# Performance work log

Hardware: AMD Instinct MI355X
Metric: run time of the kernel (lower is better)

## Reference

```python
import jax, jax.numpy as jnp
import numpy as np

NUM_GROUPS = 64  # matches fill_max of ids; all groups present w.h.p. so unique-inverse == ids


def setup_inputs() -> dict:
    key = jax.random.key(0)
    ks = jax.random.split(key, 8)
    B, N, D = 8, 8192, 512
    s = 1.0 / np.sqrt(D)
    return {
        "x": jax.random.normal(ks[0], (B, N, D), dtype=jnp.float32),
        "ids": jax.random.randint(ks[1], (N,), 0, NUM_GROUPS),
        "w1": jax.random.normal(ks[2], (D, D), dtype=jnp.float32) * s,
        "b1": jax.random.normal(ks[3], (D,), dtype=jnp.float32) * s,
        "w2": jax.random.normal(ks[4], (D, D), dtype=jnp.float32) * s,
        "b2": jax.random.normal(ks[5], (D,), dtype=jnp.float32) * s,
        "w3": jax.random.normal(ks[6], (D, D), dtype=jnp.float32) * s,
        "b3": jax.random.normal(ks[7], (D,), dtype=jnp.float32) * s,
    }


def reference(x, ids, w1, b1, w2, b2, w3, b3):
    # x: [B, N, D]; ids: [N] group labels in [0, NUM_GROUPS)
    G = NUM_GROUPS
    a = jnp.einsum('bnd,ed->bne', x, w1) + b1          # linear1 logits
    v = jnp.einsum('bnd,ed->bne', x, w2) + b2          # linear2 values
    # move segment axis to front: [N, B, D]
    aT = jnp.transpose(a, (1, 0, 2))
    vT = jnp.transpose(v, (1, 0, 2))
    # per-group stable softmax along the segment axis
    mx = jax.lax.stop_gradient(jax.ops.segment_max(aT, ids, num_segments=G))  # [G,B,D]
    ex = jnp.exp(aT - mx[ids])
    denom = jax.ops.segment_sum(ex, ids, num_segments=G)                      # [G,B,D]
    wts = ex / denom[ids]                                                     # [N,B,D]
    # weighted scatter-sum of values -> [G, B, D] -> [B, G, D]
    y = jnp.transpose(jax.ops.segment_sum(vT * wts, ids, num_segments=G), (1, 0, 2))
    out = jnp.einsum('bgd,ed->bge', y, w3) + b3        # linear3
    # expand: gather group outputs back to per-element rows -> [B, N, D]
    return out[:, ids]
```

## Files before the change

kernel.cpp:

```cpp
#include <hip/hip_runtime.h>
#include <hip/hip_bf16.h>
#include <math.h>

#define B_ 8
#define N_ 8192
#define D_ 512
#define G_ 64
#define M_ (B_ * N_)

typedef short bf16x8 __attribute__((ext_vector_type(8)));
typedef float f32x4 __attribute__((ext_vector_type(4)));

__device__ __forceinline__ unsigned short f2bf(float f) {
    __hip_bfloat16 h = __float2bfloat16(f);
    return *reinterpret_cast<unsigned short*>(&h);
}
__device__ __forceinline__ void gload_lds16(const void* g, void* l) {
    __builtin_amdgcn_global_load_lds((const __attribute__((address_space(1))) void*)g,
                                     (__attribute__((address_space(3))) void*)l,
                                     16, 0, 0);
}

__global__ __launch_bounds__(256) void cast_xp(const float* __restrict__ x,
                                               const int* __restrict__ perm,
                                               unsigned short* __restrict__ xb) {
    const int total = M_ * 128;
    for (int idx = blockIdx.x * 256 + threadIdx.x; idx < total;
         idx += gridDim.x * 256) {
        const int row = idx >> 7;
        const int q = (idx & 127) * 4;
        const int b = row >> 13;
        const int i = row & 8191;
        const float* src = x + (((size_t)(b << 13) + perm[i]) << 9) + q;
        float4 f = *(const float4*)src;
        ushort4 u;
        u.x = f2bf(f.x); u.y = f2bf(f.y); u.z = f2bf(f.z); u.w = f2bf(f.w);
        *(ushort4*)(xb + ((size_t)row << 9) + q) = u;
    }
}

__global__ __launch_bounds__(256) void cast_w(const float* __restrict__ w1,
                                              const float* __restrict__ b1,
                                              const float* __restrict__ w2,
                                              const float* __restrict__ b2,
                                              unsigned short* __restrict__ wB,
                                              float* __restrict__ biasB) {
    int t = blockIdx.x * 256 + threadIdx.x;
    int idx = t * 4;
    int row = idx >> 9;
    int col = idx & 511;
    const float* src = (row < 512) ? (w1 + (size_t)row * 512 + col)
                                   : (w2 + (size_t)(row - 512) * 512 + col);
    float4 f = *(const float4*)src;
    ushort4 u;
    u.x = f2bf(f.x); u.y = f2bf(f.y); u.z = f2bf(f.z); u.w = f2bf(f.w);
    *(ushort4*)(wB + idx) = u;
    if (t < 1024) biasB[t] = (t < 512) ? b1[t] : b2[t - 512];
}

__global__ __launch_bounds__(256) void bl_hist(const int* __restrict__ ids,
                                               int* __restrict__ counts,
                                               int* __restrict__ stripbase) {
    __shared__ int sid[N_];
    __shared__ int sc[256];
    const int g = blockIdx.x;
    const int t = threadIdx.x;
    for (int i = t; i < N_; i += 256) sid[i] = ids[i];
    __syncthreads();
    int c = 0;
    const int nb = t * 32;
#pragma unroll 8
    for (int k = 0; k < 32; ++k) c += (sid[nb + k] == g) ? 1 : 0;
    sc[t] = c;
    __syncthreads();
    if (t == 0) {
        int run = 0;
        for (int i = 0; i < 256; ++i) { int v = sc[i]; sc[i] = run; run += v; }
        counts[g] = run;
    }
    __syncthreads();
    stripbase[g * 256 + t] = sc[t];
}

__global__ __launch_bounds__(256) void bl_emit(const int* __restrict__ ids,
                                               const int* __restrict__ counts,
                                               const int* __restrict__ stripbase,
                                               int* __restrict__ baseO,
                                               int* __restrict__ fgO,
                                               int* __restrict__ perm) {
    __shared__ int sid[N_];
    __shared__ int sb[G_ + 1];
    __shared__ int sbs;
    const int g = blockIdx.x;
    const int t = threadIdx.x;
    for (int i = t; i < N_; i += 256) sid[i] = ids[i];
    if (t == 0) {
        int a = 0;
        for (int gg = 0; gg < G_; ++gg) { sb[gg] = a; a += counts[gg]; }
        sb[G_] = a;
        sbs = sb[g];
    }
    __syncthreads();
    if (g == 0 && t < G_) {
        baseO[t] = sb[t];
        const int row = t * 128;
        int gg = 0;
        while (gg + 1 < G_ && sb[gg + 1] <= row) ++gg;
        fgO[t] = gg;
    }
    int pos = sbs + stripbase[g * 256 + t];
    const int nb = t * 32;
    for (int k = 0; k < 32; ++k)
        if (sid[nb + k] == g) perm[pos++] = nb + k;
}

__global__ __launch_bounds__(512, 2) void gemm_fused(const unsigned short* __restrict__ xb,
                                                     const unsigned short* __restrict__ wB,
                                                     const float* __restrict__ biasB,
                                                     const int* __restrict__ base,
                                                     const int* __restrict__ fg,
                                                     float* __restrict__ pt) {
    extern __shared__ unsigned short smem[];
    unsigned short* lsA = smem;
    unsigned short* lsB = smem + 32768;

    const int o  = blockIdx.x;
    const int mt = (o & 7) + ((o >> 5) << 3);
    const int nt = (o >> 3) & 3;
    const int b  = mt >> 5;
    const int tlb = (mt & 31) * 2;
    const int c0 = nt * 128;

    const int tid = threadIdx.x;
    const int l = tid & 63;
    const int w = tid >> 6;
    const int wm = w >> 2;
    const int wn = w & 3;
    const int lr = l >> 3;
    const int lslot = l & 7;
    const int fr = l & 15;
    const int kq = l >> 4;
    const int scol = 8 * (lslot ^ lr);

    f32x4 acc[8][4];
#pragma unroll
    for (int i = 0; i < 8; ++i)
#pragma unroll
        for (int j = 0; j < 4; ++j) acc[i][j] = (f32x4){0.f, 0.f, 0.f, 0.f};

    const size_t abase = (((size_t)b << 13) + (size_t)(mt & 31) * 256) << 9;

    auto stageT = [&](int buf, int kt) {
#pragma unroll
        for (int q = 0; q < 4; ++q) {
            const int c = w * 4 + q;
            const int row = c * 8 + lr;
            gload_lds16(xb + abase + ((size_t)row << 9) + kt + scol,
                        lsA + buf * 16384 + c * 512);
        }
#pragma unroll
        for (int q = 0; q < 4; ++q) {
            const int c = w * 4 + q;
            const int srcrow = ((c >> 2) & 1) * 512 + c0 + (c >> 3) * 32
                             + (c & 3) * 8 + lr;
            gload_lds16(wB + ((size_t)srcrow << 9) + kt + scol,
                        lsB + buf * 16384 + c * 512);
        }
    };

    stageT(0, 0);
    __syncthreads();
    int cur = 0;
    for (int t8 = 0; t8 < 8; ++t8) {
        if (t8 < 7) stageT(cur ^ 1, (t8 + 1) * 64);
        const unsigned short* pA = lsA + cur * 16384;
        const unsigned short* pB = lsB + cur * 16384;
        const int ib0 = 8 * (kq ^ (fr & 7));
        const int ib1 = 8 * ((4 + kq) ^ (fr & 7));
        bf16x8 bq0[4], bq1[4];
#pragma unroll
        for (int j = 0; j < 4; ++j) {
            const int brow = (wn * 64 + j * 16 + fr) * 64;
            bq0[j] = *(const bf16x8*)&pB[brow + ib0];
            bq1[j] = *(const bf16x8*)&pB[brow + ib1];
        }
#pragma unroll
        for (int i = 0; i < 8; ++i) {
            const int arow = (wm * 128 + i * 16 + fr) * 64;
            bf16x8 a0 = *(const bf16x8*)&pA[arow + ib0];
            bf16x8 a1 = *(const bf16x8*)&pA[arow + ib1];
#pragma unroll
            for (int j = 0; j < 4; ++j)
                acc[i][j] = __builtin_amdgcn_mfma_f32_16x16x32_bf16(a0, bq0[j], acc[i][j], 0, 0, 0);
#pragma unroll
            for (int j = 0; j < 4; ++j)
                acc[i][j] = __builtin_amdgcn_mfma_f32_16x16x32_bf16(a1, bq1[j], acc[i][j], 0, 0, 0);
        }
        __syncthreads();
        cur ^= 1;
    }

    const int tl = tlb + wm;
    const int fg0 = fg[tl];
    const int bnd0 = (fg0 + 1 < G_) ? base[fg0 + 1] : (1 << 30);
    const int bnd1 = (fg0 + 2 < G_) ? base[fg0 + 2] : (1 << 30);
    const int bnd2 = (fg0 + 3 < G_) ? base[fg0 + 3] : (1 << 30);
    float b1c[2], b2c[2];
#pragma unroll
    for (int j = 0; j < 2; ++j) {
        const int col = c0 + wn * 32 + j * 16 + fr;
        b1c[j] = biasB[col];
        b2c[j] = biasB[512 + col];
    }
    float dp[4][2] = {}, yp[4][2] = {};
    const int rbase = tl * 128 + kq * 4;
#pragma unroll
    for (int i = 0; i < 8; ++i)
#pragma unroll
        for (int rr = 0; rr < 4; ++rr) {
            const int row = rbase + i * 16 + rr;
            const int s = (row >= bnd0) + (row >= bnd1) + (row >= bnd2);
#pragma unroll
            for (int j = 0; j < 2; ++j) {
                const float e = __expf(acc[i][j][rr] + b1c[j]);
                const float ey = e * (acc[i][j + 2][rr] + b2c[j]);
#pragma unroll
                for (int s2 = 0; s2 < 4; ++s2) {
                    dp[s2][j] += (s == s2) ? e : 0.f;
                    yp[s2][j] += (s == s2) ? ey : 0.f;
                }
            }
        }
#pragma unroll
    for (int s2 = 0; s2 < 4; ++s2)
#pragma unroll
        for (int j = 0; j < 2; ++j) {
            dp[s2][j] += __shfl_xor(dp[s2][j], 16);
            dp[s2][j] += __shfl_xor(dp[s2][j], 32);
            yp[s2][j] += __shfl_xor(yp[s2][j], 16);
            yp[s2][j] += __shfl_xor(yp[s2][j], 32);
        }
    if (kq == 0) {
#pragma unroll
        for (int s2 = 0; s2 < 4; ++s2)
#pragma unroll
            for (int j = 0; j < 2; ++j) {
                const int colp = c0 + wn * 32 + j * 16 + fr;
                float2 v = make_float2(dp[s2][j], yp[s2][j]);
                *(float2*)&pt[(((size_t)(b * 64 + tl) * 4 + s2) * 512 + colp) * 2] = v;
            }
    }
}

__global__ __launch_bounds__(256) void combineC(const float* __restrict__ pt,
                                                const int* __restrict__ base,
                                                const int* __restrict__ counts,
                                                const int* __restrict__ fg,
                                                float* __restrict__ y) {
    const int g = blockIdx.x, b = blockIdx.y;
    const int bs = base[g];
    int cnt = counts[g];
    if (cnt == 0) cnt = 1;
    const int t0 = bs >> 7, t1 = (bs + cnt - 1) >> 7;
    for (int c = threadIdx.x; c < 512; c += 256) {
        float d = 0.f, yy = 0.f;
        for (int t = t0; t <= t1; ++t) {
            const int s = g - fg[t];
            if (s >= 0 && s < 4) {
                const float* p = &pt[((((size_t)(b * 64 + t)) * 4 + s) * 512 + c) * 2];
                d += p[0];
                yy += p[1];
            }
        }
        y[((size_t)(b * G_ + g)) * 512 + c] = yy / d;
    }
}

__global__ __launch_bounds__(256) void gemm3(const float* __restrict__ y,
                                             const float* __restrict__ w3,
                                             const float* __restrict__ b3,
                                             float* __restrict__ out_small) {
    __shared__ float ys[16][68];
    __shared__ float wss[16][68];
    const int m0 = blockIdx.x * 64;
    const int n0 = blockIdx.y * 64;
    const int tid = threadIdx.x;
    const int tr = tid >> 4;
    const int tc = tid & 15;
    const int lrow = tid >> 2;
    const int lk4 = (tid & 3) * 4;

    float acc[4][4] = {};

    for (int k0 = 0; k0 < D_; k0 += 16) {
        float4 yv = *(const float4*)(y + (size_t)(m0 + lrow) * D_ + k0 + lk4);
        float4 wv = *(const float4*)(w3 + (size_t)(n0 + lrow) * D_ + k0 + lk4);
        __syncthreads();
        ys[lk4 + 0][lrow] = yv.x;  ys[lk4 + 1][lrow] = yv.y;
        ys[lk4 + 2][lrow] = yv.z;  ys[lk4 + 3][lrow] = yv.w;
        wss[lk4 + 0][lrow] = wv.x; wss[lk4 + 1][lrow] = wv.y;
        wss[lk4 + 2][lrow] = wv.z; wss[lk4 + 3][lrow] = wv.w;
        __syncthreads();
#pragma unroll
        for (int kk = 0; kk < 16; ++kk) {
            float4 y4 = *(const float4*)&ys[kk][tr * 4];
            float4 w4 = *(const float4*)&wss[kk][tc * 4];
            float ya[4] = {y4.x, y4.y, y4.z, y4.w};
            float wa[4] = {w4.x, w4.y, w4.z, w4.w};
#pragma unroll
            for (int i = 0; i < 4; ++i)
#pragma unroll
                for (int j = 0; j < 4; ++j)
                    acc[i][j] = fmaf(ya[i], wa[j], acc[i][j]);
        }
    }

    float bb[4];
#pragma unroll
    for (int j = 0; j < 4; ++j) bb[j] = b3[n0 + tc * 4 + j];
#pragma unroll
    for (int i = 0; i < 4; ++i) {
        size_t o = (size_t)(m0 + tr * 4 + i) * D_ + n0 + tc * 4;
        float4 r;
        r.x = acc[i][0] + bb[0]; r.y = acc[i][1] + bb[1];
        r.z = acc[i][2] + bb[2]; r.w = acc[i][3] + bb[3];
        *(float4*)(out_small + o) = r;
    }
}

__global__ __launch_bounds__(256) void gather_out(const int* __restrict__ ids,
                                                  const float* __restrict__ out_small,
                                                  float* __restrict__ out) {
    const int c = blockIdx.x * 256 + threadIdx.x;
    const int per_row = D_ / 4;
    const int b = c / (N_ * per_row);
    const int rem = c % (N_ * per_row);
    const int n = rem / per_row;
    const int q = rem % per_row;
    const int g = ids[n];
    float4 val = *(const float4*)(out_small + ((size_t)b * G_ + g) * D_ + q * 4);
    *(float4*)(out + (size_t)c * 4) = val;
}

extern "C" void kernel_launch(void* const* d_in, const int* in_sizes, int n_in,
                              void* d_out, int out_size, void* d_ws, size_t ws_size,
                              hipStream_t stream) {
    (void)in_sizes; (void)n_in; (void)out_size; (void)ws_size;
    const float* x   = (const float*)d_in[0];
    const int*   ids = (const int*)d_in[1];
    const float* w1  = (const float*)d_in[2];
    const float* b1  = (const float*)d_in[3];
    const float* w2  = (const float*)d_in[4];
    const float* b2  = (const float*)d_in[5];
    const float* w3  = (const float*)d_in[6];
    const float* b3  = (const float*)d_in[7];
    float* out = (float*)d_out;

    float* ws_f = (float*)d_ws;
    unsigned short* xb = (unsigned short*)ws_f;
    float* after_xb  = ws_f + 16777216;
    unsigned short* wB = (unsigned short*)after_xb;
    float* biasB     = after_xb + 262144;
    float* pt        = biasB + 1024;
    float* y         = pt + 2097152;
    float* out_small = y + 262144;
    int*   perm      = (int*)(out_small + 262144);
    int*   base      = perm + N_;
    int*   counts    = base + G_;
    int*   fg        = counts + G_;
    int*   stripbase = fg + G_;

    hipFuncSetAttribute((const void*)gemm_fused,
                        hipFuncAttributeMaxDynamicSharedMemorySize, 131072);

    hipLaunchKernelGGL(bl_hist, dim3(G_), dim3(256), 0, stream, ids, counts, stripbase);
    hipLaunchKernelGGL(bl_emit, dim3(G_), dim3(256), 0, stream,
                       ids, counts, stripbase, base, fg, perm);
    hipLaunchKernelGGL(cast_w, dim3(512), dim3(256), 0, stream, w1, b1, w2, b2, wB, biasB);
    hipLaunchKernelGGL(cast_xp, dim3(2048), dim3(256), 0, stream, x, perm, xb);
    hipLaunchKernelGGL(gemm_fused, dim3(1024), dim3(512), 131072, stream,
                       xb, wB, biasB, base, fg, pt);
    hipLaunchKernelGGL(combineC, dim3(G_, B_), dim3(256), 0, stream, pt, base, counts, fg, y);
    hipLaunchKernelGGL(gemm3, dim3(8, 8), dim3(256), 0, stream, y, w3, b3, out_small);
    hipLaunchKernelGGL(gather_out, dim3(32768), dim3(256), 0, stream, ids, out_small, out);
}
```

Baseline: 194.9 us.

## Restructure GEMM main loop into ping-pong schedule with explicit vmcnt waits

```diff
diff --git a/kernel.cpp b/kernel.cpp
--- a/kernel.cpp
+++ b/kernel.cpp
@@ -150,13 +150,13 @@
 
     const size_t abase = (((size_t)b << 13) + (size_t)(mt & 31) * 256) << 9;
 
-    auto stageT = [&](int buf, int kt) {
+    auto stage8 = [&](int slot, int kt) {
 #pragma unroll
         for (int q = 0; q < 4; ++q) {
             const int c = w * 4 + q;
             const int row = c * 8 + lr;
             gload_lds16(xb + abase + ((size_t)row << 9) + kt + scol,
-                        lsA + buf * 16384 + c * 512);
+                        lsA + slot * 16384 + c * 512);
         }
 #pragma unroll
         for (int q = 0; q < 4; ++q) {
@@ -164,40 +164,56 @@
             const int srcrow = ((c >> 2) & 1) * 512 + c0 + (c >> 3) * 32
                              + (c & 3) * 8 + lr;
             gload_lds16(wB + ((size_t)srcrow << 9) + kt + scol,
-                        lsB + buf * 16384 + c * 512);
+                        lsB + slot * 16384 + c * 512);
         }
     };
 
-    stageT(0, 0);
-    __syncthreads();
-    int cur = 0;
-    for (int t8 = 0; t8 < 8; ++t8) {
-        if (t8 < 7) stageT(cur ^ 1, (t8 + 1) * 64);
-        const unsigned short* pA = lsA + cur * 16384;
-        const unsigned short* pB = lsB + cur * 16384;
-        const int ib0 = 8 * (kq ^ (fr & 7));
-        const int ib1 = 8 * ((4 + kq) ^ (fr & 7));
-        bf16x8 bq0[4], bq1[4];
-#pragma unroll
-        for (int j = 0; j < 4; ++j) {
-            const int brow = (wn * 64 + j * 16 + fr) * 64;
-            bq0[j] = *(const bf16x8*)&pB[brow + ib0];
-            bq1[j] = *(const bf16x8*)&pB[brow + ib1];
-        }
-#pragma unroll
-        for (int i = 0; i < 8; ++i) {
-            const int arow = (wm * 128 + i * 16 + fr) * 64;
-            bf16x8 a0 = *(const bf16x8*)&pA[arow + ib0];
-            bf16x8 a1 = *(const bf16x8*)&pA[arow + ib1];
-#pragma unroll
-            for (int j = 0; j < 4; ++j)
-                acc[i][j] = __builtin_amdgcn_mfma_f32_16x16x32_bf16(a0, bq0[j], acc[i][j], 0, 0, 0);
-#pragma unroll
-            for (int j = 0; j < 4; ++j)
-                acc[i][j] = __builtin_amdgcn_mfma_f32_16x16x32_bf16(a1, bq1[j], acc[i][j], 0, 0, 0);
-        }
-        __syncthreads();
-        cur ^= 1;
+    stage8(0, 0);
+    stage8(1, 64);
+
+    for (int i4 = 0; i4 < 4; ++i4) {
+#pragma unroll
+        for (int half = 0; half < 2; ++half) {
+            const int slot = half;
+            const bool doStage = (half == 0) ? (i4 > 0) : (i4 < 3);
+            if (doStage) stage8(1 - half, (2 * i4 + 1 + half) * 64);
+            if (doStage || (half == 0)) {
+                asm volatile("s_waitcnt vmcnt(8)" ::: "memory");
+            } else {
+                asm volatile("s_waitcnt vmcnt(0)" ::: "memory");
+            }
+            __builtin_amdgcn_s_barrier();
+
+            const unsigned short* pA = lsA + slot * 16384;
+            const unsigned short* pB = lsB + slot * 16384;
+            bf16x8 bq[4];
+#pragma unroll
+            for (int ks = 0; ks < 2; ++ks) {
+                const int ib = 8 * ((ks * 4 + kq) ^ (fr & 7));
+#pragma unroll
+                for (int ih = 0; ih < 2; ++ih) {
+                    bf16x8 a[4];
+#pragma unroll
+                    for (int i = 0; i < 4; ++i)
+                        a[i] = *(const bf16x8*)&pA[(wm * 128 + (ih * 4 + i) * 16 + fr) * 64 + ib];
+                    if (ih == 0) {
+#pragma unroll
+                        for (int j = 0; j < 4; ++j)
+                            bq[j] = *(const bf16x8*)&pB[(wn * 64 + j * 16 + fr) * 64 + ib];
+                    }
+                    __builtin_amdgcn_s_barrier();
+                    __builtin_amdgcn_s_setprio(1);
+#pragma unroll
+                    for (int i = 0; i < 4; ++i)
+#pragma unroll
+                        for (int j = 0; j < 4; ++j)
+                            acc[ih * 4 + i][j] = __builtin_amdgcn_mfma_f32_16x16x32_bf16(
+                                a[i], bq[j], acc[ih * 4 + i][j], 0, 0, 0);
+                    __builtin_amdgcn_s_setprio(0);
+                    __builtin_amdgcn_s_barrier();
+                }
+            }
+        }
     }
 
     const int tl = tlb + wm;
```

After: 204.6 us. +5.0%, slower.
